# Kernel tuning notes

Measured on AMD Instinct MI355X. Metric: run time of the kernel, lower is better.

## Reference

```python
import jax, jax.numpy as jnp
import numpy as np

KS = 5
NF = 64
B, H, W = 2, 160, 160


def _conv1x1(x, w, b):
    # x: (B,Ci,H,W), w: (Co,Ci)
    return jnp.einsum('oi,bihw->bohw', w, x) + b[None, :, None, None]


def _conv2x2(x, w, b, dil):
    # x: (B,1,Hp,Wp), w: (64,1,2,2); VALID conv with dilation dil
    y = jax.lax.conv_general_dilated(x, w, (1, 1), 'VALID',
                                     rhs_dilation=(dil, dil),
                                     dimension_numbers=('NCHW', 'OIHW', 'NCHW'))
    return y + b[None, :, None, None]


def _conv_s(x, w, b):
    # conv1 module, mode 's': gather taps (0,0),(1,1),(1,2),(2,1) of each 3x3 patch,
    # then (1,4) conv == linear combo of 4 shifted images.
    h = x.shape[2] - 2
    wd = x.shape[3] - 2
    x0 = x[:, 0]
    taps = jnp.stack([x0[:, 0:h, 0:wd],
                      x0[:, 1:h + 1, 1:wd + 1],
                      x0[:, 1:h + 1, 2:wd + 2],
                      x0[:, 2:h + 2, 1:wd + 1]], axis=1)  # (B,4,h,wd)
    return jnp.einsum('ok,bkhw->bohw', w.reshape(NF, 4), taps) + b[None, :, None, None]


def _construct(c, dense_ps):
    # relu then dense 1x1-conv chain with channel concat, final 1x1 -> 4 channels
    x = jax.nn.relu(c)
    for (wt, bs) in dense_ps[:-1]:
        feat = jax.nn.relu(_conv1x1(x, wt, bs))
        x = jnp.concatenate([x, feat], axis=1)
    wt, bs = dense_ps[-1]
    return _conv1x1(x, wt, bs)


def _ag(x, sigx, sigy, theta, sigr):
    # x: (B,ks,ks,HW); params: (B,HW). Per-pixel anisotropic bilateral kernel.
    ks = x.shape[1]
    r = jnp.arange(ks, dtype=x.dtype) - ks // 2
    sq = (r[:, None] ** 2 + r[None, :] ** 2)[None, :, :, None]  # (1,ks,ks,1)
    sx = sigx[:, None, None, :]
    sy = sigy[:, None, None, :]
    th = theta[:, None, None, :]
    sr = sigr[:, None, None, :]
    spatial = jnp.exp(-sq / (2.0 * sr ** 2))
    disx = jnp.abs(x[:, ks // 2:ks // 2 + 1] - x)       # center row
    disy = jnp.abs(x[:, :, ks // 2:ks // 2 + 1] - x)    # center col
    a = sx * disx
    bb = sy * disy
    color = jnp.exp(-0.5 * (a ** 2 - 2.0 * th * a * bb + bb ** 2))
    kern = spatial * color
    kern = kern / jnp.sum(kern, axis=(1, 2), keepdims=True)
    return jnp.sum(kern * x, axis=(1, 2))  # (B,HW)


def _forward(x_in, conv1x_w, conv1x_b, conv1c_w, conv1c_b, conv1cs_w, conv1cs_b,
             w2, b2, w3, b3, w4, b4, w5, b5, w6, b6):
    dense_ps = [(w2, b2), (w3, b3), (w4, b4), (w5, b5), (w6, b6)]

    def fk(x, mod):
        if mod == 's':
            c = _conv_s(x, conv1cs_w, conv1cs_b)
        elif mod == 'c':
            c = _conv2x2(x, conv1c_w, conv1c_b, 2)
        else:
            c = _conv2x2(x, conv1x_w, conv1x_b, 1)
        return _construct(c, dense_ps)

    def mode_ens(x, p, mod):
        pad = lambda z: jnp.pad(z, ((0, 0), (0, 0), (0, p), (0, p)), mode='reflect')
        r0 = fk(pad(x), mod)
        r2 = jnp.rot90(fk(pad(jnp.rot90(x, 2, (2, 3))), mod), 2, (2, 3))
        r1 = jnp.rot90(fk(pad(jnp.rot90(x, 1, (2, 3))), mod), 3, (2, 3))
        r3 = jnp.rot90(fk(pad(jnp.rot90(x, 3, (2, 3))), mod), 1, (2, 3))
        return (r0 + r2) / 2.0, (r1 + r3) / 2.0

    e1x, e2x = mode_ens(x_in, 1, 'x')
    e1s, e2s = mode_ens(x_in, 2, 's')
    e1c, e2c = mode_ens(x_in, 2, 'c')
    par = (e1x + e2x + e1s + e2s + e1c + e2c) / 6.0  # (B,4,H,W)

    b, c, h, w = x_in.shape
    sigx = jnp.clip(jax.nn.sigmoid(par[:, 0]).reshape(b, -1) + 1e-6, 0.0, 1.0)
    sigy = jnp.clip(jax.nn.sigmoid(par[:, 1]).reshape(b, -1) + 1e-6, 0.0, 1.0)
    theta = jnp.clip(jnp.tanh(par[:, 2]).reshape(b, -1), -1.0, 1.0)
    sigr = jnp.clip(jnp.tanh(par[:, 3]).reshape(b, -1) + 1e-6, -1.0, 1.0)

    ph = KS // 2
    xt = jnp.pad(x_in, ((0, 0), (0, 0), (ph, ph), (ph, ph)))  # zero pad
    # unfold -> (B, KS, KS, H*W)
    patches = jnp.stack([jnp.stack([xt[:, 0, i:i + h, j:j + w].reshape(b, -1)
                                    for j in range(KS)], axis=1)
                         for i in range(KS)], axis=1)
    outs = _ag(patches, sigx * 20.0, sigy * 20.0, theta, sigr * 10.0 + 10.0).reshape(b, c, h, w)
    return outs, sigx, sigy, theta, sigr


def setup_inputs() -> dict:
    key = jax.random.key(0)
    k = jax.random.split(key, 10)
    def kn(kk, shape, fan_in):
        return jax.random.normal(kk, shape, jnp.float32) * np.float32(np.sqrt(2.0 / fan_in))
    zb = lambda n: jnp.zeros((n,), jnp.float32)
    return {
        'x_in': jax.random.normal(k[0], (B, 1, H, W), jnp.float32),
        'conv1x_w': kn(k[1], (NF, 1, 2, 2), 4), 'conv1x_b': zb(NF),
        'conv1c_w': kn(k[2], (NF, 1, 2, 2), 4), 'conv1c_b': zb(NF),
        'conv1cs_w': kn(k[3], (NF, 1, 1, 4), 4), 'conv1cs_b': zb(NF),
        'w2': kn(k[4], (NF, NF), NF), 'b2': zb(NF),
        'w3': kn(k[5], (NF, 2 * NF), 2 * NF), 'b3': zb(NF),
        'w4': kn(k[6], (NF, 3 * NF), 3 * NF), 'b4': zb(NF),
        'w5': kn(k[7], (NF, 4 * NF), 4 * NF), 'b5': zb(NF),
        'w6': kn(k[8], (4, 5 * NF), 5 * NF), 'b6': zb(4),
    }


def reference(x_in, conv1x_w, conv1x_b, conv1c_w, conv1c_b, conv1cs_w, conv1cs_b,
              w2, b2, w3, b3, w4, b4, w5, b5, w6, b6):
    return _forward(x_in, conv1x_w, conv1x_b, conv1c_w, conv1c_b, conv1cs_w, conv1cs_b,
                    w2, b2, w3, b3, w4, b4, w5, b5, w6, b6)
```

## Files before the change

kernel.cpp:

```cpp
#include <hip/hip_runtime.h>
#include <hip/hip_bf16.h>
#include <math.h>
#include <string.h>


#define NN   160
#define NPIX 25600

typedef __attribute__((ext_vector_type(4))) float float4v;
typedef __attribute__((ext_vector_type(8))) unsigned short ushort8;
typedef __attribute__((ext_vector_type(2))) unsigned int uint2v;
typedef __attribute__((ext_vector_type(4))) unsigned int uint4v;
typedef __attribute__((ext_vector_type(8))) __bf16 bf16x8;

#define PINV(x) asm volatile("" : "+v"(x))

__device__ __forceinline__ int refp(int a) { return (a <= NN - 1) ? a : (2 * (NN - 1) - a); }

__device__ __forceinline__ unsigned int pk2(float lo, float hi) {
    float2 f; f.x = lo; f.y = hi;
    __hip_bfloat162 h = __float22bfloat162_rn(f);
    unsigned int u;
    memcpy(&u, &h, 4);
    return u;
}
__device__ __forceinline__ ushort8 cvt8(const float* __restrict__ p) {
    const float4v f0 = *(const float4v*)p;
    const float4v f1 = *(const float4v*)(p + 4);
    uint4v u;
    u[0] = pk2(f0[0], f0[1]); u[1] = pk2(f0[2], f0[3]);
    u[2] = pk2(f1[0], f1[1]); u[3] = pk2(f1[2], f1[3]);
    return __builtin_bit_cast(ushort8, u);
}

template <int NCH>
__device__ __forceinline__ void dense_layer(const ushort8 (&A)[NCH], float4v biasv,
                                            unsigned short* Xs, int w, int lo16, int lq) {
    const int K = NCH * 32;
#pragma unroll
    for (int pp = 0; pp < 2; ++pp) {
        const int px0 = (pp * 2) * 16 + lo16;
        const int px1 = (pp * 2 + 1) * 16 + lo16;
        float4v acc0 = biasv, acc1 = biasv;
#pragma unroll
        for (int s = 0; s < NCH; ++s) {
            const int c8 = s * 4 + lq;
            const bf16x8 bf0 = __builtin_bit_cast(bf16x8, *(const ushort8*)&Xs[c8 * 512 + px0 * 8]);
            const bf16x8 bf1 = __builtin_bit_cast(bf16x8, *(const ushort8*)&Xs[c8 * 512 + px1 * 8]);
            const bf16x8 af  = __builtin_bit_cast(bf16x8, A[s]);
            acc0 = __builtin_amdgcn_mfma_f32_16x16x32_bf16(af, bf0, acc0, 0, 0, 0);
            acc1 = __builtin_amdgcn_mfma_f32_16x16x32_bf16(af, bf1, acc1, 0, 0, 0);
        }
        const int cb = K + w * 16 + lq * 4;
        uint2v o0, o1;
        o0[0] = pk2(fmaxf(acc0[0], 0.0f), fmaxf(acc0[1], 0.0f));
        o0[1] = pk2(fmaxf(acc0[2], 0.0f), fmaxf(acc0[3], 0.0f));
        o1[0] = pk2(fmaxf(acc1[0], 0.0f), fmaxf(acc1[1], 0.0f));
        o1[1] = pk2(fmaxf(acc1[2], 0.0f), fmaxf(acc1[3], 0.0f));
        *(uint2v*)&Xs[(cb >> 3) * 512 + px0 * 8 + (cb & 7)] = o0;
        *(uint2v*)&Xs[(cb >> 3) * 512 + px1 * 8 + (cb & 7)] = o1;
    }
    __syncthreads();
}

__global__
__attribute__((amdgpu_flat_work_group_size(256, 256)))
__attribute__((amdgpu_waves_per_eu(3, 3)))
void bnet_mlp_kernel(
    const float* __restrict__ x,
    const float* __restrict__ wx, const float* __restrict__ bx,
    const float* __restrict__ wcs, const float* __restrict__ bcs,
    const float* __restrict__ wc, const float* __restrict__ bc,
    const float* __restrict__ w2, const float* __restrict__ b2,
    const float* __restrict__ w3, const float* __restrict__ b3,
    const float* __restrict__ w4, const float* __restrict__ b4,
    const float* __restrict__ w5, const float* __restrict__ b5,
    const float* __restrict__ w6,
    float* __restrict__ par)
{
    __shared__ unsigned short Xs[20480];
    __shared__ unsigned short Ac[1536];
    float* red = (float*)Xs;

    const int t = threadIdx.x;
    const int lane = t & 63;
    const int lo16 = lane & 15;
    const int lq = lane >> 4;
    const int w = __builtin_amdgcn_readfirstlane(t >> 6);

    if (t < 192) {
        const int m = t >> 6, ch = t & 63;
        const float* w1m = (m == 0) ? wx : (m == 1) ? wcs : wc;
        const float4v wv = *(const float4v*)&w1m[ch * 4];
        uint4v o;
        o[0] = pk2(wv[0], wv[1]); o[1] = pk2(wv[2], wv[3]);
        o[2] = 0u; o[3] = 0u;
        *(uint4v*)&Ac[((m * 4 + (ch >> 4)) * 16 + (ch & 15)) * 8] = o;
    }

    const int arow = w * 16 + lo16;
    ushort8 a2[2], a3[4], a4[6], a5[8], a6[3];
#pragma unroll
    for (int s = 0; s < 2; ++s) { a2[s] = cvt8(&w2[arow * 64 + s * 32 + lq * 8]);  PINV(a2[s]); }
#pragma unroll
    for (int s = 0; s < 4; ++s) { a3[s] = cvt8(&w3[arow * 128 + s * 32 + lq * 8]); PINV(a3[s]); }
#pragma unroll
    for (int s = 0; s < 6; ++s) { a4[s] = cvt8(&w4[arow * 192 + s * 32 + lq * 8]); PINV(a4[s]); }
#pragma unroll
    for (int s = 0; s < 8; ++s) { a5[s] = cvt8(&w5[arow * 256 + s * 32 + lq * 8]); PINV(a5[s]); }
#pragma unroll
    for (int c = 0; c < 3; ++c) {
        const int ch = (3 * w + c) * 32;
        if (ch < 320 && lo16 < 4) {
            a6[c] = cvt8(&w6[lo16 * 320 + ch + lq * 8]);
        } else {
            ushort8 z = {0, 0, 0, 0, 0, 0, 0, 0};
            a6[c] = z;
        }
        PINV(a6[c]);
    }
    const float4v b2v = *(const float4v*)&b2[w * 16 + lq * 4];
    const float4v b3v = *(const float4v*)&b3[w * 16 + lq * 4];
    const float4v b4v = *(const float4v*)&b4[w * 16 + lq * 4];
    const float4v b5v = *(const float4v*)&b5[w * 16 + lq * 4];

    const int bid = blockIdx.x;
    const int nit = 12 + (bid < 384 ? 1 : 0);
    const int g0  = (bid < 384) ? bid * 13 : bid * 12 + 384;

    float4v acc6[4];
    int cur_tb = -1;

    for (int it = 0; it < nit; ++it) {
        const int g = g0 + it;
        const int v = g % 12;
        const int tb = g / 12;
        const int tile = tb >> 1;
        const int b = tb & 1;
        const int mode = v >> 2;
        const int k = v & 3;

        __syncthreads();

        if (tb != cur_tb) {
            if (cur_tb >= 0) {
                const int ftile = cur_tb >> 1;
                const int fb = cur_tb & 1;
                if (lq == 0) {
#pragma unroll
                    for (int pt = 0; pt < 4; ++pt)
                        *(float4v*)&red[(((w * 4) + pt) * 16 + lo16) * 4] = acc6[pt];
                }
                __syncthreads();
                if (w == 0) {
                    float4v sv;
#pragma unroll
                    for (int r = 0; r < 4; ++r)
                        sv[r] = red[(((0 * 4) + lq) * 16 + lo16) * 4 + r]
                              + red[(((1 * 4) + lq) * 16 + lo16) * 4 + r]
                              + red[(((2 * 4) + lq) * 16 + lo16) * 4 + r]
                              + red[(((3 * 4) + lq) * 16 + lo16) * 4 + r];
                    const int pixg = ftile * 64 + lq * 16 + lo16;
#pragma unroll
                    for (int r = 0; r < 4; ++r)
                        atomicAdd(&par[(r * 2 + fb) * NPIX + pixg], sv[r]);
                }
                __syncthreads();
            }
#pragma unroll
            for (int pt = 0; pt < 4; ++pt) { float4v z = {0.f, 0.f, 0.f, 0.f}; acc6[pt] = z; }
            cur_tb = tb;
        }

        const float* xb = x + b * NPIX;
        const float* b1 = (mode == 0) ? bx : (mode == 1) ? bcs : bc;

        int dy, dx;
        if (mode == 0)      { dy = lq >> 1;        dx = lq & 1; }
        else if (mode == 1) { dy = (lq == 0) ? 0 : (lq == 3) ? 2 : 1;
                              dx = (lq == 0) ? 0 : (lq == 2) ? 2 : 1; }
        else                { dy = (lq >> 1) * 2;  dx = (lq & 1) * 2; }

        const int gpix = tile * 64 + w * 16 + lo16;
        const int gpi = gpix / NN;
        const int gpj = gpix - gpi * NN;
        int rr, cc;
        if (k == 0)      { rr = refp(gpi + dy); cc = refp(gpj + dx); }
        else if (k == 1) { rr = refp(gpi + dx); cc = (gpj >= dy) ? (gpj - dy) : (dy - gpj); }
        else if (k == 2) { rr = (gpi >= dy) ? (gpi - dy) : (dy - gpi);
                           cc = (gpj >= dx) ? (gpj - dx) : (dx - gpj); }
        else             { rr = (gpi >= dx) ? (gpi - dx) : (dx - gpi); cc = refp(gpj + dy); }
        const float gval = xb[rr * NN + cc];

        const float tv0 = __shfl(gval, 0 * 16 + lo16);
        const float tv1 = __shfl(gval, 1 * 16 + lo16);
        const float tv2 = __shfl(gval, 2 * 16 + lo16);
        const float tv3 = __shfl(gval, 3 * 16 + lo16);
        uint4v bu;
        bu[0] = pk2(tv0, tv1); bu[1] = pk2(tv2, tv3); bu[2] = 0u; bu[3] = 0u;
        if (lq != 0) { bu[0] = 0u; bu[1] = 0u; }
        const bf16x8 bfrag = __builtin_bit_cast(bf16x8, bu);

#pragma unroll
        for (int ot = 0; ot < 4; ++ot) {
            uint4v au = *(const uint4v*)&Ac[((mode * 4 + ot) * 16 + lo16) * 8];
            if (lq != 0) { au[0] = 0u; au[1] = 0u; au[2] = 0u; au[3] = 0u; }
            const bf16x8 afrag = __builtin_bit_cast(bf16x8, au);
            float4v acc = *(const float4v*)&b1[ot * 16 + lq * 4];
            acc = __builtin_amdgcn_mfma_f32_16x16x32_bf16(afrag, bfrag, acc, 0, 0, 0);
            const int cb = ot * 16 + lq * 4;
            const int px = w * 16 + lo16;
            uint2v o;
            o[0] = pk2(fmaxf(acc[0], 0.0f), fmaxf(acc[1], 0.0f));
            o[1] = pk2(fmaxf(acc[2], 0.0f), fmaxf(acc[3], 0.0f));
            *(uint2v*)&Xs[(cb >> 3) * 512 + px * 8 + (cb & 7)] = o;
        }
        __syncthreads();

        dense_layer<2>(a2, b2v, Xs, w, lo16, lq);
        dense_layer<4>(a3, b3v, Xs, w, lo16, lq);
        dense_layer<6>(a4, b4v, Xs, w, lo16, lq);
        dense_layer<8>(a5, b5v, Xs, w, lo16, lq);

#pragma unroll
        for (int pt = 0; pt < 4; ++pt) {
            const int px = pt * 16 + lo16;
#pragma unroll
            for (int c = 0; c < 3; ++c) {
                int chb = (3 * w + c) * 32;
                chb = (chb < 288) ? chb : 288;
                const int c8 = (chb >> 3) + lq;
                const bf16x8 bf = __builtin_bit_cast(
                    bf16x8, *(const ushort8*)&Xs[c8 * 512 + px * 8]);
                acc6[pt] = __builtin_amdgcn_mfma_f32_16x16x32_bf16(
                    __builtin_bit_cast(bf16x8, a6[c]), bf, acc6[pt], 0, 0, 0);
            }
        }
    }

    __syncthreads();
    {
        const int ftile = cur_tb >> 1;
        const int fb = cur_tb & 1;
        if (lq == 0) {
#pragma unroll
            for (int pt = 0; pt < 4; ++pt)
                *(float4v*)&red[(((w * 4) + pt) * 16 + lo16) * 4] = acc6[pt];
        }
        __syncthreads();
        if (w == 0) {
            float4v sv;
#pragma unroll
            for (int r = 0; r < 4; ++r)
                sv[r] = red[(((0 * 4) + lq) * 16 + lo16) * 4 + r]
                      + red[(((1 * 4) + lq) * 16 + lo16) * 4 + r]
                      + red[(((2 * 4) + lq) * 16 + lo16) * 4 + r]
                      + red[(((3 * 4) + lq) * 16 + lo16) * 4 + r];
            const int pixg = ftile * 64 + lq * 16 + lo16;
#pragma unroll
            for (int r = 0; r < 4; ++r)
                atomicAdd(&par[(r * 2 + fb) * NPIX + pixg], sv[r]);
        }
    }
}

__global__ __launch_bounds__(64) void bnet_bilateral_kernel(
    const float* __restrict__ x, const float* __restrict__ b6,
    float* __restrict__ out)
{
    const int tid = blockIdx.x * 64 + threadIdx.x;
    const int b = tid / NPIX;
    const int pix = tid - b * NPIX;
    const int pi = pix / NN;
    const int pj = pix - pi * NN;

    float* par = out + 2 * NPIX;
    const float inv12 = 1.0f / 12.0f;
    const float p0 = par[(0 + b) * NPIX + pix] * inv12 + b6[0];
    const float p1 = par[(2 + b) * NPIX + pix] * inv12 + b6[1];
    const float p2 = par[(4 + b) * NPIX + pix] * inv12 + b6[2];
    const float p3 = par[(6 + b) * NPIX + pix] * inv12 + b6[3];

    float sigx = 1.0f / (1.0f + __expf(-p0)) + 1e-6f;
    sigx = fminf(fmaxf(sigx, 0.0f), 1.0f);
    float sigy = 1.0f / (1.0f + __expf(-p1)) + 1e-6f;
    sigy = fminf(fmaxf(sigy, 0.0f), 1.0f);
    float t2 = __expf(2.0f * fminf(fmaxf(p2, -15.0f), 15.0f));
    float th = (t2 - 1.0f) / (t2 + 1.0f);
    th = fminf(fmaxf(th, -1.0f), 1.0f);
    float t3 = __expf(2.0f * fminf(fmaxf(p3, -15.0f), 15.0f));
    float sigr = (t3 - 1.0f) / (t3 + 1.0f) + 1e-6f;
    sigr = fminf(fmaxf(sigr, -1.0f), 1.0f);

    par[(0 + b) * NPIX + pix] = sigx;
    par[(2 + b) * NPIX + pix] = sigy;
    par[(4 + b) * NPIX + pix] = th;
    par[(6 + b) * NPIX + pix] = sigr;

    const float sx = sigx * 20.0f;
    const float sy = sigy * 20.0f;
    const float sr = sigr * 10.0f + 10.0f;

    const float* xb = x + b * NPIX;
    float patch[5][5];
#pragma unroll
    for (int ky = 0; ky < 5; ++ky) {
#pragma unroll
        for (int kx = 0; kx < 5; ++kx) {
            const int r = pi + ky - 2, c = pj + kx - 2;
            patch[ky][kx] = (r >= 0 && r < NN && c >= 0 && c < NN) ? xb[r * NN + c] : 0.0f;
        }
    }

    const float inv2sr2 = 1.0f / (2.0f * sr * sr);
    float num = 0.0f, den = 0.0f;
#pragma unroll
    for (int ky = 0; ky < 5; ++ky) {
#pragma unroll
        for (int kx = 0; kx < 5; ++kx) {
            const float v = patch[ky][kx];
            const float dxv = fabsf(patch[2][kx] - v);
            const float dyv = fabsf(patch[ky][2] - v);
            const float a = sx * dxv;
            const float bb = sy * dyv;
            const float sq = (float)((ky - 2) * (ky - 2) + (kx - 2) * (kx - 2));
            const float kern = __expf(-sq * inv2sr2 - 0.5f * (a * a - 2.0f * th * a * bb + bb * bb));
            den += kern;
            num = fmaf(kern, v, num);
        }
    }
    out[tid] = num / den;
}

extern "C" void kernel_launch(void* const* d_in, const int* in_sizes, int n_in,
                              void* d_out, int out_size, void* d_ws, size_t ws_size,
                              hipStream_t stream) {
    const float* x   = (const float*)d_in[0];
    const float* wx  = (const float*)d_in[1];
    const float* bx  = (const float*)d_in[2];
    const float* wc  = (const float*)d_in[3];
    const float* bc  = (const float*)d_in[4];
    const float* wcs = (const float*)d_in[5];
    const float* bcs = (const float*)d_in[6];
    const float* w2  = (const float*)d_in[7];
    const float* b2  = (const float*)d_in[8];
    const float* w3  = (const float*)d_in[9];
    const float* b3  = (const float*)d_in[10];
    const float* w4  = (const float*)d_in[11];
    const float* b4  = (const float*)d_in[12];
    const float* w5  = (const float*)d_in[13];
    const float* b5  = (const float*)d_in[14];
    const float* w6  = (const float*)d_in[15];
    const float* b6  = (const float*)d_in[16];
    float* out = (float*)d_out;

    (void)hipMemsetAsync(out + 2 * NPIX, 0, 8 * NPIX * sizeof(float), stream);

    hipLaunchKernelGGL(bnet_mlp_kernel, dim3(768), dim3(256), 0, stream,
                       x, wx, bx, wcs, bcs, wc, bc,
                       w2, b2, w3, b3, w4, b4, w5, b5, w6,
                       out + 2 * NPIX);

    hipLaunchKernelGGL(bnet_bilateral_kernel, dim3(800), dim3(64), 0, stream,
                       x, b6, out);
}
```

Before: 171.1 us.

## Give each wave its own pixels and stream pre-packed bf16 weights from a workspace

Weights are now converted to bf16 MFMA fragment layout once by a new prep kernel and read from global or L2 in each layer, instead of staying resident in registers. The work split changes from output-channel-split waves sharing 64 pixels to each wave owning 16 pixels and computing all output channels. That removes all per-layer __syncthreads and the shared-memory cross-wave reduction of the final layer, and the atomics are issued directly per wave. In exchange every wave re-reads weight fragments from memory each iteration, adding a small extra kernel launch and more load traffic.

```diff
diff --git a/kernel.cpp b/kernel.cpp
--- a/kernel.cpp
+++ b/kernel.cpp
@@ -6,14 +6,19 @@
 
 #define NN   160
 #define NPIX 25600
+
+#define W2OFF 0
+#define W3OFF 512
+#define W4OFF 1536
+#define W5OFF 3072
+#define W6OFF 5120
+#define WSUNITS 5888
 
 typedef __attribute__((ext_vector_type(4))) float float4v;
 typedef __attribute__((ext_vector_type(8))) unsigned short ushort8;
 typedef __attribute__((ext_vector_type(2))) unsigned int uint2v;
 typedef __attribute__((ext_vector_type(4))) unsigned int uint4v;
 typedef __attribute__((ext_vector_type(8))) __bf16 bf16x8;
-
-#define PINV(x) asm volatile("" : "+v"(x))
 
 __device__ __forceinline__ int refp(int a) { return (a <= NN - 1) ? a : (2 * (NN - 1) - a); }
 
@@ -24,43 +29,71 @@
     memcpy(&u, &h, 4);
     return u;
 }
-__device__ __forceinline__ ushort8 cvt8(const float* __restrict__ p) {
-    const float4v f0 = *(const float4v*)p;
-    const float4v f1 = *(const float4v*)(p + 4);
-    uint4v u;
-    u[0] = pk2(f0[0], f0[1]); u[1] = pk2(f0[2], f0[3]);
-    u[2] = pk2(f1[0], f1[1]); u[3] = pk2(f1[2], f1[3]);
-    return __builtin_bit_cast(ushort8, u);
+
+__global__ __launch_bounds__(256) void bnet_prep_kernel(
+    const float* __restrict__ w2, const float* __restrict__ w3,
+    const float* __restrict__ w4, const float* __restrict__ w5,
+    const float* __restrict__ w6, ushort8* __restrict__ ws)
+{
+    const int u = blockIdx.x * 256 + threadIdx.x;
+    const int lq = u & 3;
+    float src[8];
+    if (u < W6OFF) {
+        const float* wp; int K, rel;
+        if (u < W3OFF)      { wp = w2; K = 64;  rel = u; }
+        else if (u < W4OFF) { wp = w3; K = 128; rel = u - W3OFF; }
+        else if (u < W5OFF) { wp = w4; K = 192; rel = u - W4OFF; }
+        else                { wp = w5; K = 256; rel = u - W5OFF; }
+        const int arow = (rel >> 2) & 63;
+        const int s = rel >> 8;
+        const float* p = &wp[arow * K + s * 32 + lq * 8];
+#pragma unroll
+        for (int e = 0; e < 8; ++e) src[e] = p[e];
+    } else {
+        const int rel = u - W6OFF;
+        const int r = (rel >> 2) & 15;
+        const int c = rel >> 6;
+        if (r < 4 && c < 10) {
+            const float* p = &w6[r * 320 + c * 32 + lq * 8];
+#pragma unroll
+            for (int e = 0; e < 8; ++e) src[e] = p[e];
+        } else {
+#pragma unroll
+            for (int e = 0; e < 8; ++e) src[e] = 0.0f;
+        }
+    }
+    uint4v o;
+    o[0] = pk2(src[0], src[1]); o[1] = pk2(src[2], src[3]);
+    o[2] = pk2(src[4], src[5]); o[3] = pk2(src[6], src[7]);
+    ws[u] = __builtin_bit_cast(ushort8, o);
 }
 
 template <int NCH>
-__device__ __forceinline__ void dense_layer(const ushort8 (&A)[NCH], float4v biasv,
-                                            unsigned short* Xs, int w, int lo16, int lq) {
+__device__ __forceinline__ void dense_all(const ushort8* __restrict__ wsL,
+                                          const float* __restrict__ bL,
+                                          unsigned short* Xs, int px, int lo16, int lq) {
     const int K = NCH * 32;
-#pragma unroll
-    for (int pp = 0; pp < 2; ++pp) {
-        const int px0 = (pp * 2) * 16 + lo16;
-        const int px1 = (pp * 2 + 1) * 16 + lo16;
-        float4v acc0 = biasv, acc1 = biasv;
-#pragma unroll
-        for (int s = 0; s < NCH; ++s) {
-            const int c8 = s * 4 + lq;
-            const bf16x8 bf0 = __builtin_bit_cast(bf16x8, *(const ushort8*)&Xs[c8 * 512 + px0 * 8]);
-            const bf16x8 bf1 = __builtin_bit_cast(bf16x8, *(const ushort8*)&Xs[c8 * 512 + px1 * 8]);
-            const bf16x8 af  = __builtin_bit_cast(bf16x8, A[s]);
-            acc0 = __builtin_amdgcn_mfma_f32_16x16x32_bf16(af, bf0, acc0, 0, 0, 0);
-            acc1 = __builtin_amdgcn_mfma_f32_16x16x32_bf16(af, bf1, acc1, 0, 0, 0);
-        }
-        const int cb = K + w * 16 + lq * 4;
-        uint2v o0, o1;
-        o0[0] = pk2(fmaxf(acc0[0], 0.0f), fmaxf(acc0[1], 0.0f));
-        o0[1] = pk2(fmaxf(acc0[2], 0.0f), fmaxf(acc0[3], 0.0f));
-        o1[0] = pk2(fmaxf(acc1[0], 0.0f), fmaxf(acc1[1], 0.0f));
-        o1[1] = pk2(fmaxf(acc1[2], 0.0f), fmaxf(acc1[3], 0.0f));
-        *(uint2v*)&Xs[(cb >> 3) * 512 + px0 * 8 + (cb & 7)] = o0;
-        *(uint2v*)&Xs[(cb >> 3) * 512 + px1 * 8 + (cb & 7)] = o1;
-    }
-    __syncthreads();
+    float4v acc[4];
+#pragma unroll
+    for (int ot = 0; ot < 4; ++ot) acc[ot] = *(const float4v*)&bL[ot * 16 + lq * 4];
+#pragma unroll
+    for (int s = 0; s < NCH; ++s) {
+        const bf16x8 bf = __builtin_bit_cast(
+            bf16x8, *(const ushort8*)&Xs[(s * 4 + lq) * 512 + px * 8]);
+#pragma unroll
+        for (int ot = 0; ot < 4; ++ot) {
+            const bf16x8 af = __builtin_bit_cast(bf16x8, wsL[(s * 64 + ot * 16 + lo16) * 4 + lq]);
+            acc[ot] = __builtin_amdgcn_mfma_f32_16x16x32_bf16(af, bf, acc[ot], 0, 0, 0);
+        }
+    }
+#pragma unroll
+    for (int ot = 0; ot < 4; ++ot) {
+        const int cb = K + ot * 16 + lq * 4;
+        uint2v o;
+        o[0] = pk2(fmaxf(acc[ot][0], 0.0f), fmaxf(acc[ot][1], 0.0f));
+        o[1] = pk2(fmaxf(acc[ot][2], 0.0f), fmaxf(acc[ot][3], 0.0f));
+        *(uint2v*)&Xs[(cb >> 3) * 512 + px * 8 + (cb & 7)] = o;
+    }
 }
 
 __global__
@@ -71,22 +104,20 @@
     const float* __restrict__ wx, const float* __restrict__ bx,
     const float* __restrict__ wcs, const float* __restrict__ bcs,
     const float* __restrict__ wc, const float* __restrict__ bc,
-    const float* __restrict__ w2, const float* __restrict__ b2,
-    const float* __restrict__ w3, const float* __restrict__ b3,
-    const float* __restrict__ w4, const float* __restrict__ b4,
-    const float* __restrict__ w5, const float* __restrict__ b5,
-    const float* __restrict__ w6,
+    const float* __restrict__ b2, const float* __restrict__ b3,
+    const float* __restrict__ b4, const float* __restrict__ b5,
+    const ushort8* __restrict__ wsb,
     float* __restrict__ par)
 {
     __shared__ unsigned short Xs[20480];
     __shared__ unsigned short Ac[1536];
-    float* red = (float*)Xs;
 
     const int t = threadIdx.x;
     const int lane = t & 63;
     const int lo16 = lane & 15;
     const int lq = lane >> 4;
     const int w = __builtin_amdgcn_readfirstlane(t >> 6);
+    const int px = w * 16 + lo16;
 
     if (t < 192) {
         const int m = t >> 6, ch = t & 63;
@@ -97,38 +128,13 @@
         o[2] = 0u; o[3] = 0u;
         *(uint4v*)&Ac[((m * 4 + (ch >> 4)) * 16 + (ch & 15)) * 8] = o;
     }
-
-    const int arow = w * 16 + lo16;
-    ushort8 a2[2], a3[4], a4[6], a5[8], a6[3];
-#pragma unroll
-    for (int s = 0; s < 2; ++s) { a2[s] = cvt8(&w2[arow * 64 + s * 32 + lq * 8]);  PINV(a2[s]); }
-#pragma unroll
-    for (int s = 0; s < 4; ++s) { a3[s] = cvt8(&w3[arow * 128 + s * 32 + lq * 8]); PINV(a3[s]); }
-#pragma unroll
-    for (int s = 0; s < 6; ++s) { a4[s] = cvt8(&w4[arow * 192 + s * 32 + lq * 8]); PINV(a4[s]); }
-#pragma unroll
-    for (int s = 0; s < 8; ++s) { a5[s] = cvt8(&w5[arow * 256 + s * 32 + lq * 8]); PINV(a5[s]); }
-#pragma unroll
-    for (int c = 0; c < 3; ++c) {
-        const int ch = (3 * w + c) * 32;
-        if (ch < 320 && lo16 < 4) {
-            a6[c] = cvt8(&w6[lo16 * 320 + ch + lq * 8]);
-        } else {
-            ushort8 z = {0, 0, 0, 0, 0, 0, 0, 0};
-            a6[c] = z;
-        }
-        PINV(a6[c]);
-    }
-    const float4v b2v = *(const float4v*)&b2[w * 16 + lq * 4];
-    const float4v b3v = *(const float4v*)&b3[w * 16 + lq * 4];
-    const float4v b4v = *(const float4v*)&b4[w * 16 + lq * 4];
-    const float4v b5v = *(const float4v*)&b5[w * 16 + lq * 4];
+    __syncthreads();
 
     const int bid = blockIdx.x;
     const int nit = 12 + (bid < 384 ? 1 : 0);
     const int g0  = (bid < 384) ? bid * 13 : bid * 12 + 384;
 
-    float4v acc6[4];
+    float4v acc6 = {0.f, 0.f, 0.f, 0.f};
     int cur_tb = -1;
 
     for (int it = 0; it < nit; ++it) {
@@ -140,35 +146,18 @@
         const int mode = v >> 2;
         const int k = v & 3;
 
-        __syncthreads();
-
         if (tb != cur_tb) {
             if (cur_tb >= 0) {
                 const int ftile = cur_tb >> 1;
                 const int fb = cur_tb & 1;
                 if (lq == 0) {
-#pragma unroll
-                    for (int pt = 0; pt < 4; ++pt)
-                        *(float4v*)&red[(((w * 4) + pt) * 16 + lo16) * 4] = acc6[pt];
+                    const int pixg = ftile * 64 + px;
+#pragma unroll
+                    for (int r = 0; r < 4; ++r)
+                        atomicAdd(&par[(r * 2 + fb) * NPIX + pixg], acc6[r]);
                 }
-                __syncthreads();
-                if (w == 0) {
-                    float4v sv;
-#pragma unroll
-                    for (int r = 0; r < 4; ++r)
-                        sv[r] = red[(((0 * 4) + lq) * 16 + lo16) * 4 + r]
-                              + red[(((1 * 4) + lq) * 16 + lo16) * 4 + r]
-                              + red[(((2 * 4) + lq) * 16 + lo16) * 4 + r]
-                              + red[(((3 * 4) + lq) * 16 + lo16) * 4 + r];
-                    const int pixg = ftile * 64 + lq * 16 + lo16;
-#pragma unroll
-                    for (int r = 0; r < 4; ++r)
-                        atomicAdd(&par[(r * 2 + fb) * NPIX + pixg], sv[r]);
-                }
-                __syncthreads();
+                float4v z = {0.f, 0.f, 0.f, 0.f}; acc6 = z;
             }
-#pragma unroll
-            for (int pt = 0; pt < 4; ++pt) { float4v z = {0.f, 0.f, 0.f, 0.f}; acc6[pt] = z; }
             cur_tb = tb;
         }
 
@@ -181,7 +170,7 @@
                               dx = (lq == 0) ? 0 : (lq == 2) ? 2 : 1; }
         else                { dy = (lq >> 1) * 2;  dx = (lq & 1) * 2; }
 
-        const int gpix = tile * 64 + w * 16 + lo16;
+        const int gpix = tile * 64 + px;
         const int gpi = gpix / NN;
         const int gpj = gpix - gpi * NN;
         int rr, cc;
@@ -209,57 +198,34 @@
             float4v acc = *(const float4v*)&b1[ot * 16 + lq * 4];
             acc = __builtin_amdgcn_mfma_f32_16x16x32_bf16(afrag, bfrag, acc, 0, 0, 0);
             const int cb = ot * 16 + lq * 4;
-            const int px = w * 16 + lo16;
             uint2v o;
             o[0] = pk2(fmaxf(acc[0], 0.0f), fmaxf(acc[1], 0.0f));
             o[1] = pk2(fmaxf(acc[2], 0.0f), fmaxf(acc[3], 0.0f));
             *(uint2v*)&Xs[(cb >> 3) * 512 + px * 8 + (cb & 7)] = o;
         }
-        __syncthreads();
-
-        dense_layer<2>(a2, b2v, Xs, w, lo16, lq);
-        dense_layer<4>(a3, b3v, Xs, w, lo16, lq);
-        dense_layer<6>(a4, b4v, Xs, w, lo16, lq);
-        dense_layer<8>(a5, b5v, Xs, w, lo16, lq);
-
-#pragma unroll
-        for (int pt = 0; pt < 4; ++pt) {
-            const int px = pt * 16 + lo16;
-#pragma unroll
-            for (int c = 0; c < 3; ++c) {
-                int chb = (3 * w + c) * 32;
-                chb = (chb < 288) ? chb : 288;
-                const int c8 = (chb >> 3) + lq;
-                const bf16x8 bf = __builtin_bit_cast(
-                    bf16x8, *(const ushort8*)&Xs[c8 * 512 + px * 8]);
-                acc6[pt] = __builtin_amdgcn_mfma_f32_16x16x32_bf16(
-                    __builtin_bit_cast(bf16x8, a6[c]), bf, acc6[pt], 0, 0, 0);
-            }
-        }
-    }
-
-    __syncthreads();
+
+        dense_all<2>(wsb + W2OFF, b2, Xs, px, lo16, lq);
+        dense_all<4>(wsb + W3OFF, b3, Xs, px, lo16, lq);
+        dense_all<6>(wsb + W4OFF, b4, Xs, px, lo16, lq);
+        dense_all<8>(wsb + W5OFF, b5, Xs, px, lo16, lq);
+
+#pragma unroll
+        for (int c = 0; c < 10; ++c) {
+            const bf16x8 bf = __builtin_bit_cast(
+                bf16x8, *(const ushort8*)&Xs[(c * 4 + lq) * 512 + px * 8]);
+            const bf16x8 af = __builtin_bit_cast(bf16x8, wsb[W6OFF + (c * 16 + lo16) * 4 + lq]);
+            acc6 = __builtin_amdgcn_mfma_f32_16x16x32_bf16(af, bf, acc6, 0, 0, 0);
+        }
+    }
+
     {
         const int ftile = cur_tb >> 1;
         const int fb = cur_tb & 1;
         if (lq == 0) {
-#pragma unroll
-            for (int pt = 0; pt < 4; ++pt)
-                *(float4v*)&red[(((w * 4) + pt) * 16 + lo16) * 4] = acc6[pt];
-        }
-        __syncthreads();
-        if (w == 0) {
-            float4v sv;
+            const int pixg = ftile * 64 + px;
 #pragma unroll
             for (int r = 0; r < 4; ++r)
-                sv[r] = red[(((0 * 4) + lq) * 16 + lo16) * 4 + r]
-                      + red[(((1 * 4) + lq) * 16 + lo16) * 4 + r]
-                      + red[(((2 * 4) + lq) * 16 + lo16) * 4 + r]
-                      + red[(((3 * 4) + lq) * 16 + lo16) * 4 + r];
-            const int pixg = ftile * 64 + lq * 16 + lo16;
-#pragma unroll
-            for (int r = 0; r < 4; ++r)
-                atomicAdd(&par[(r * 2 + fb) * NPIX + pixg], sv[r]);
+                atomicAdd(&par[(r * 2 + fb) * NPIX + pixg], acc6[r]);
         }
     }
 }
@@ -353,12 +319,16 @@
     const float* w6  = (const float*)d_in[15];
     const float* b6  = (const float*)d_in[16];
     float* out = (float*)d_out;
+    ushort8* ws = (ushort8*)d_ws;
 
     (void)hipMemsetAsync(out + 2 * NPIX, 0, 8 * NPIX * sizeof(float), stream);
+
+    hipLaunchKernelGGL(bnet_prep_kernel, dim3(WSUNITS / 256), dim3(256), 0, stream,
+                       w2, w3, w4, w5, w6, ws);
 
     hipLaunchKernelGGL(bnet_mlp_kernel, dim3(768), dim3(256), 0, stream,
                        x, wx, bx, wcs, bcs, wc, bc,
-                       w2, b2, w3, b3, w4, b4, w5, b5, w6,
+                       b2, b3, b4, b5, (const ushort8*)ws,
                        out + 2 * NPIX);
 
     hipLaunchKernelGGL(bnet_bilateral_kernel, dim3(800), dim3(64), 0, stream,
```

Measured after the change: 446.8 us. +161.1%, slower.
